# Optimization experiments

Measured on AMD Instinct MI355X. Metric: run time of the kernel, lower is better.

Reference implementation:

```python
import jax, jax.numpy as jnp
import numpy as np

N = 100000      # num nodes
E = 1600000     # num edges
F_IN = 128
F_OUT = 128
BN_EPS = 1e-5


def setup_inputs() -> dict:
    key = jax.random.key(0)
    ks = jax.random.split(key, 8)
    x = jax.random.normal(ks[0], (N, F_IN), dtype=jnp.float32)
    edge_index = jax.random.randint(ks[1], (2, E), 0, N, dtype=jnp.int64)
    # GIN learnable epsilon (init 0.0)
    eps = jnp.zeros((), dtype=jnp.float32)
    # MLP: Linear(F_IN->F_OUT) -> BatchNorm1d -> ReLU -> Linear(F_OUT->F_OUT)
    lim1 = 1.0 / np.sqrt(F_IN)
    W1 = jax.random.uniform(ks[2], (F_OUT, F_IN), minval=-lim1, maxval=lim1, dtype=jnp.float32)
    b1 = jax.random.uniform(ks[3], (F_OUT,), minval=-lim1, maxval=lim1, dtype=jnp.float32)
    gamma = jnp.ones((F_OUT,), dtype=jnp.float32)
    beta = jnp.zeros((F_OUT,), dtype=jnp.float32)
    lim2 = 1.0 / np.sqrt(F_OUT)
    W2 = jax.random.uniform(ks[4], (F_OUT, F_OUT), minval=-lim2, maxval=lim2, dtype=jnp.float32)
    b2 = jax.random.uniform(ks[5], (F_OUT,), minval=-lim2, maxval=lim2, dtype=jnp.float32)
    return {"x": x, "edge_index": edge_index, "eps": eps,
            "W1": W1, "b1": b1, "gamma": gamma, "beta": beta,
            "W2": W2, "b2": b2}


def reference(x, edge_index, eps, W1, b1, gamma, beta, W2, b2):
    row, col = edge_index[0], edge_index[1]
    # gather neighbor features and scatter-add into destination nodes
    agg = jax.ops.segment_sum(x[col], row, num_segments=x.shape[0])  # [N, F_IN]
    h = (1.0 + eps) * x + agg
    # Linear 1
    h = h @ W1.T + b1  # [N, F_OUT]
    # BatchNorm1d (training mode: batch stats over nodes, biased variance)
    mu = jnp.mean(h, axis=0)
    var = jnp.mean(jnp.square(h - mu), axis=0)
    h = (h - mu) * jax.lax.rsqrt(var + BN_EPS) * gamma + beta
    h = jax.nn.relu(h)
    # Linear 2
    return h @ W2.T + b2
```

## Files before the change

### kernel.cpp

```cpp
#include <hip/hip_runtime.h>


#define F 128
#define NPB 64

typedef __attribute__((ext_vector_type(8))) short short8;
typedef __attribute__((ext_vector_type(4))) float float4v;

__device__ inline float b2f(unsigned short u) {
    union { unsigned int i; float f; } v; v.i = ((unsigned int)u) << 16; return v.f;
}
__device__ inline unsigned short f2b(float f) {
    union { float f; unsigned int i; } v; v.f = f;
    unsigned int r = v.i + 0x7FFFu + ((v.i >> 16) & 1u);
    return (unsigned short)(r >> 16);
}

__global__ __launch_bounds__(256) void conv_kernel(const float* __restrict__ x,
                                                   unsigned short* __restrict__ xh, int total,
                                                   const float* __restrict__ W1,
                                                   const float* __restrict__ W2,
                                                   unsigned short* __restrict__ w1h,
                                                   unsigned short* __restrict__ w2h,
                                                   int* __restrict__ bucketCnt, int nbuk,
                                                   float* __restrict__ stats) {
    int t = blockIdx.x * 256 + threadIdx.x;
    int i = t * 8;
    if (i < total) {
        float4 v0 = *(const float4*)(x + i);
        float4 v1 = *(const float4*)(x + i + 4);
        short8 o;
        o[0] = (short)f2b(v0.x); o[1] = (short)f2b(v0.y); o[2] = (short)f2b(v0.z); o[3] = (short)f2b(v0.w);
        o[4] = (short)f2b(v1.x); o[5] = (short)f2b(v1.y); o[6] = (short)f2b(v1.z); o[7] = (short)f2b(v1.w);
        *(short8*)(xh + i) = o;
    }
    if (t < F * F) {
        w1h[t] = f2b(W1[t]);
        w2h[t] = f2b(W2[t]);
    }
    if (blockIdx.x == 0) {
        for (int k = threadIdx.x; k < nbuk; k += 256) bucketCnt[k] = 0;
    } else if (blockIdx.x == 1) {
        if (threadIdx.x < 256) stats[threadIdx.x] = 0.f;
    }
}

__global__ __launch_bounds__(256) void bucket_hist_kernel(const int* __restrict__ rows,
                                                          int* __restrict__ bucketCnt,
                                                          int E, int nbuk) {
    extern __shared__ int bh[];
    int tid = threadIdx.x;
    for (int i = tid; i < nbuk; i += 256) bh[i] = 0;
    __syncthreads();
    int stride = gridDim.x * 256;
    for (int i = blockIdx.x * 256 + tid; i < E; i += stride)
        atomicAdd(&bh[rows[i] >> 6], 1);
    __syncthreads();
    for (int b = tid; b < nbuk; b += 256) {
        int c = bh[b];
        if (c) atomicAdd(&bucketCnt[b], c);
    }
}

__global__ void scan_buckets_kernel(const int* __restrict__ bucketCnt, int* __restrict__ bOffs,
                                    int* __restrict__ gcursor, int nbuk) {
    const int SEG = 7;
    __shared__ int tmp[256];
    int t = threadIdx.x;
    int base = t * SEG;
    int v[SEG], s = 0;
#pragma unroll
    for (int j = 0; j < SEG; j++) {
        int idx = base + j;
        v[j] = (idx < nbuk) ? bucketCnt[idx] : 0;
        s += v[j];
    }
    tmp[t] = s;
    __syncthreads();
    for (int off = 1; off < 256; off <<= 1) {
        int u = (t >= off) ? tmp[t - off] : 0;
        __syncthreads();
        tmp[t] += u;
        __syncthreads();
    }
    int run = tmp[t] - s;
#pragma unroll
    for (int j = 0; j < SEG; j++) {
        int idx = base + j;
        if (idx < nbuk) { bOffs[idx] = run; gcursor[idx] = run; }
        run += v[j];
    }
    if (t == 255) bOffs[nbuk] = tmp[255];
}

__global__ __launch_bounds__(1024) void binned_scatter_kernel(const int* __restrict__ rows,
                                                              const int* __restrict__ cols,
                                                              int* __restrict__ gcursor,
                                                              int* __restrict__ recbuf,
                                                              int E, int nbuk) {
    extern __shared__ int sm[];
    int* bh = sm;
    int* gb = sm + nbuk;
    int tid = threadIdx.x;
    int chunk = (E + gridDim.x - 1) / gridDim.x;
    int e0 = blockIdx.x * chunk;
    int e1 = min(E, e0 + chunk);
    for (int i = tid; i < nbuk; i += 1024) bh[i] = 0;
    __syncthreads();
    for (int i = e0 + tid; i < e1; i += 1024)
        atomicAdd(&bh[rows[i] >> 6], 1);
    __syncthreads();
    for (int b = tid; b < nbuk; b += 1024) {
        int c = bh[b];
        gb[b] = c ? atomicAdd(&gcursor[b], c) : 0;
        bh[b] = 0;
    }
    __syncthreads();
    for (int i = e0 + tid; i < e1; i += 1024) {
        int r = rows[i], c = cols[i];
        int k = r >> 6;
        int rk = atomicAdd(&bh[k], 1);
        recbuf[gb[k] + rk] = (c << 6) | (r & 63);
    }
}

__global__ __launch_bounds__(256) void bucket_sort_kernel(const int* __restrict__ recbuf,
                                                          const int* __restrict__ bOffs,
                                                          int* __restrict__ clist,
                                                          int* __restrict__ offs,
                                                          int n, int nbuk) {
    __shared__ int hist[NPB];
    __shared__ int cur[NPB];
    int b = blockIdx.x, tid = threadIdx.x;
    int base = bOffs[b];
    int cnt = bOffs[b + 1] - base;
    if (tid < NPB) hist[tid] = 0;
    __syncthreads();
    for (int i = tid; i < cnt; i += 256) atomicAdd(&hist[recbuf[base + i] & 63], 1);
    __syncthreads();
    if (tid < 64) {
        int h = hist[tid], v = h;
#pragma unroll
        for (int off = 1; off < 64; off <<= 1) {
            int u = __shfl_up(v, off, 64);
            if (tid >= off) v += u;
        }
        cur[tid] = v - h;
        int g = b * NPB + tid;
        if (g < n) offs[g] = base + v - h;
    }
    if (b == 0 && tid == 0) offs[n] = bOffs[nbuk];
    __syncthreads();
    for (int i = tid; i < cnt; i += 256) {
        int r = recbuf[base + i];
        int p = atomicAdd(&cur[r & 63], 1);
        clist[base + p] = r >> 6;
    }
}

__global__ __launch_bounds__(256) void agg_kernel(const unsigned short* __restrict__ xh,
                                                  const int* __restrict__ offs,
                                                  const int* __restrict__ clist,
                                                  const float* __restrict__ epsPtr,
                                                  unsigned short* __restrict__ h0h, int n) {
    int wave = threadIdx.x >> 6, lane = threadIdx.x & 63;
    int node = blockIdx.x * 4 + wave;
    if (node >= n) return;
    int qt = lane >> 4;
    int c16 = lane & 15;
    const short8* xh8 = (const short8*)xh;
    float acc[8];
#pragma unroll
    for (int j = 0; j < 8; j++) acc[j] = 0.f;
    int s = offs[node], e = offs[node + 1];
    int i = s;
    for (; i + 16 <= e; i += 16) {
        int c[4];
#pragma unroll
        for (int u = 0; u < 4; u++) c[u] = clist[i + 4 * u + qt];
        short8 v[4];
#pragma unroll
        for (int u = 0; u < 4; u++) v[u] = xh8[(size_t)c[u] * 16 + c16];
#pragma unroll
        for (int u = 0; u < 4; u++)
#pragma unroll
            for (int j = 0; j < 8; j++) acc[j] += b2f((unsigned short)v[u][j]);
    }
    if (i < e) {
        int c[4];
#pragma unroll
        for (int u = 0; u < 4; u++) {
            int idx = i + 4 * u + qt;
            c[u] = (idx < e) ? clist[idx] : -1;
        }
        short8 v[4];
#pragma unroll
        for (int u = 0; u < 4; u++)
            v[u] = xh8[(size_t)(c[u] < 0 ? 0 : c[u]) * 16 + c16];
#pragma unroll
        for (int u = 0; u < 4; u++) {
            if (c[u] >= 0) {
#pragma unroll
                for (int j = 0; j < 8; j++) acc[j] += b2f((unsigned short)v[u][j]);
            }
        }
    }
#pragma unroll
    for (int j = 0; j < 8; j++) {
        acc[j] += __shfl_xor(acc[j], 16, 64);
        acc[j] += __shfl_xor(acc[j], 32, 64);
    }
    if (qt == 0) {
        float sc = 1.0f + epsPtr[0];
        short8 xv = xh8[(size_t)node * 16 + c16];
        short8 o;
#pragma unroll
        for (int j = 0; j < 8; j++) {
            float r = fmaf(sc, b2f((unsigned short)xv[j]), acc[j]);
            o[j] = (short)f2b(r);
        }
        ((short8*)h0h)[(size_t)node * 16 + c16] = o;
    }
}

#define WLD 136
__global__ __launch_bounds__(256, 2) void gemm1_mfma_kernel(const unsigned short* __restrict__ h0h,
                                                            const unsigned short* __restrict__ w1h,
                                                            const float* __restrict__ b1,
                                                            unsigned short* __restrict__ h1h,
                                                            float* __restrict__ stats, int n) {
    __shared__ unsigned short wl[128 * WLD];
    __shared__ float red[4 * 256];
    int tid = threadIdx.x;
    for (int i = tid; i < 128 * 16; i += 256) {
        int r = i >> 4, ch = i & 15;
        *(short8*)(wl + r * WLD + ch * 8) = *(const short8*)(w1h + r * 128 + ch * 8);
    }
    __syncthreads();

    int wv = tid >> 6, lane = tid & 63;
    int q = lane >> 4, c15 = lane & 15;
    int rowbase = blockIdx.x * 64 + wv * 16;
    int arow = rowbase + c15; if (arow >= n) arow = n - 1;
    const unsigned short* aptr = h0h + (size_t)arow * 128 + q * 8;

    float4v acc[8];
#pragma unroll
    for (int nt = 0; nt < 8; nt++) {
        float bb = b1[nt * 16 + c15];
        acc[nt] = (float4v){bb, bb, bb, bb};
    }
#pragma unroll
    for (int ks = 0; ks < 4; ks++) {
        short8 a = *(const short8*)(aptr + ks * 32);
        const unsigned short* wp = wl + q * 8 + ks * 32;
#pragma unroll
        for (int nt = 0; nt < 8; nt++) {
            short8 b = *(const short8*)(wp + (nt * 16 + c15) * WLD);
            acc[nt] = __builtin_amdgcn_mfma_f32_16x16x32_bf16(a, b, acc[nt], 0, 0, 0);
        }
    }

    float sum[8], sq[8];
#pragma unroll
    for (int nt = 0; nt < 8; nt++) {
        sum[nt] = 0.f; sq[nt] = 0.f;
#pragma unroll
        for (int r = 0; r < 4; r++) {
            int row = rowbase + q * 4 + r;
            if (row < n) {
                float v = acc[nt][r];
                h1h[(size_t)row * 128 + nt * 16 + c15] = f2b(v);
                sum[nt] += v; sq[nt] += v * v;
            }
        }
        sum[nt] += __shfl_xor(sum[nt], 16, 64);
        sum[nt] += __shfl_xor(sum[nt], 32, 64);
        sq[nt]  += __shfl_xor(sq[nt], 16, 64);
        sq[nt]  += __shfl_xor(sq[nt], 32, 64);
    }
    if (lane < 16) {
#pragma unroll
        for (int nt = 0; nt < 8; nt++) {
            red[wv * 256 + nt * 16 + c15] = sum[nt];
            red[wv * 256 + 128 + nt * 16 + c15] = sq[nt];
        }
    }
    __syncthreads();
    if (wv == 0) {
        for (int c = lane; c < 128; c += 64) {
            float S = red[c] + red[256 + c] + red[512 + c] + red[768 + c];
            float Q = red[128 + c] + red[384 + c] + red[640 + c] + red[896 + c];
            atomicAdd(&stats[c], S);
            atomicAdd(&stats[128 + c], Q);
        }
    }
}

__global__ __launch_bounds__(256, 2) void gemm2_mfma_kernel(const unsigned short* __restrict__ h1h,
                                                            const unsigned short* __restrict__ w2h,
                                                            const float* __restrict__ b2,
                                                            const float* __restrict__ stats,
                                                            const float* __restrict__ gamma,
                                                            const float* __restrict__ beta,
                                                            float* __restrict__ out, int n) {
    __shared__ unsigned short wl[128 * WLD];
    __shared__ float ssl[256];
    int tid = threadIdx.x;
    for (int i = tid; i < 128 * 16; i += 256) {
        int r = i >> 4, ch = i & 15;
        *(short8*)(wl + r * WLD + ch * 8) = *(const short8*)(w2h + r * 128 + ch * 8);
    }
    if (tid < 128) {
        float inv_n = 1.0f / (float)n;
        float mu = stats[tid] * inv_n;
        float var = stats[F + tid] * inv_n - mu * mu;
        var = fmaxf(var, 0.0f);
        float rs = rsqrtf(var + 1e-5f);
        float s = gamma[tid] * rs;
        ssl[tid] = s;
        ssl[F + tid] = beta[tid] - mu * s;
    }
    __syncthreads();

    int wv = tid >> 6, lane = tid & 63;
    int q = lane >> 4, c15 = lane & 15;
    int rowbase = blockIdx.x * 64 + wv * 16;
    int arow = rowbase + c15; if (arow >= n) arow = n - 1;
    const unsigned short* aptr = h1h + (size_t)arow * 128 + q * 8;

    float4v acc[8];
#pragma unroll
    for (int nt = 0; nt < 8; nt++) {
        float bb = b2[nt * 16 + c15];
        acc[nt] = (float4v){bb, bb, bb, bb};
    }
#pragma unroll
    for (int ks = 0; ks < 4; ks++) {
        short8 araw = *(const short8*)(aptr + ks * 32);
        const float* ssp = ssl + ks * 32 + q * 8;
        float4 s0 = *(const float4*)(ssp);
        float4 s1 = *(const float4*)(ssp + 4);
        float4 t0 = *(const float4*)(ssp + 128);
        float4 t1 = *(const float4*)(ssp + 132);
        short8 a;
        a[0] = (short)f2b(fmaxf(fmaf(b2f((unsigned short)araw[0]), s0.x, t0.x), 0.f));
        a[1] = (short)f2b(fmaxf(fmaf(b2f((unsigned short)araw[1]), s0.y, t0.y), 0.f));
        a[2] = (short)f2b(fmaxf(fmaf(b2f((unsigned short)araw[2]), s0.z, t0.z), 0.f));
        a[3] = (short)f2b(fmaxf(fmaf(b2f((unsigned short)araw[3]), s0.w, t0.w), 0.f));
        a[4] = (short)f2b(fmaxf(fmaf(b2f((unsigned short)araw[4]), s1.x, t1.x), 0.f));
        a[5] = (short)f2b(fmaxf(fmaf(b2f((unsigned short)araw[5]), s1.y, t1.y), 0.f));
        a[6] = (short)f2b(fmaxf(fmaf(b2f((unsigned short)araw[6]), s1.z, t1.z), 0.f));
        a[7] = (short)f2b(fmaxf(fmaf(b2f((unsigned short)araw[7]), s1.w, t1.w), 0.f));
        const unsigned short* wp = wl + q * 8 + ks * 32;
#pragma unroll
        for (int nt = 0; nt < 8; nt++) {
            short8 b = *(const short8*)(wp + (nt * 16 + c15) * WLD);
            acc[nt] = __builtin_amdgcn_mfma_f32_16x16x32_bf16(a, b, acc[nt], 0, 0, 0);
        }
    }
#pragma unroll
    for (int nt = 0; nt < 8; nt++) {
#pragma unroll
        for (int r = 0; r < 4; r++) {
            int row = rowbase + q * 4 + r;
            if (row < n)
                out[(size_t)row * 128 + nt * 16 + c15] = acc[nt][r];
        }
    }
}

extern "C" void kernel_launch(void* const* d_in, const int* in_sizes, int n_in,
                              void* d_out, int out_size, void* d_ws, size_t ws_size,
                              hipStream_t stream) {
    const float* x     = (const float*)d_in[0];
    const int*   ei    = (const int*)d_in[1];
    const float* eps   = (const float*)d_in[2];
    const float* W1    = (const float*)d_in[3];
    const float* b1    = (const float*)d_in[4];
    const float* gamma = (const float*)d_in[5];
    const float* beta  = (const float*)d_in[6];
    const float* W2    = (const float*)d_in[7];
    const float* b2    = (const float*)d_in[8];
    float* out = (float*)d_out;

    const int E = in_sizes[1] / 2;
    const int n = in_sizes[0] / F;
    const int nbuk = (n + NPB - 1) / NPB;

    char* w = (char*)d_ws;
    auto alloc = [&](size_t bytes) -> void* {
        void* p = (void*)w;
        w += (bytes + 255) & ~(size_t)255;
        return p;
    };
    int*            bucketCnt = (int*)alloc((size_t)nbuk * 4);
    int*            bOffs     = (int*)alloc((size_t)(nbuk + 1) * 4);
    int*            gcursor   = (int*)alloc((size_t)nbuk * 4);
    int*            offs      = (int*)alloc((size_t)(n + 1) * 4);
    float*          stats     = (float*)alloc(256 * 4);
    unsigned short* w1h       = (unsigned short*)alloc(F * F * 2);
    unsigned short* w2h       = (unsigned short*)alloc(F * F * 2);
    int*            recbuf    = (int*)alloc((size_t)E * 4);
    int*            clist     = (int*)alloc((size_t)E * 4);
    unsigned short* xh        = (unsigned short*)alloc((size_t)n * F * 2);
    unsigned short* h0h       = (unsigned short*)alloc((size_t)n * F * 2);
    unsigned short* h1h       = (unsigned short*)alloc((size_t)n * F * 2);

    const int* rows = ei;
    const int* cols = ei + E;

    conv_kernel<<<(n * F / 8 + 255) / 256, 256, 0, stream>>>(x, xh, n * F, W1, W2, w1h, w2h,
                                                             bucketCnt, nbuk, stats);
    bucket_hist_kernel<<<256, 256, nbuk * 4, stream>>>(rows, bucketCnt, E, nbuk);
    scan_buckets_kernel<<<1, 256, 0, stream>>>(bucketCnt, bOffs, gcursor, nbuk);
    binned_scatter_kernel<<<128, 1024, nbuk * 8, stream>>>(rows, cols, gcursor, recbuf, E, nbuk);
    bucket_sort_kernel<<<nbuk, 256, 0, stream>>>(recbuf, bOffs, clist, offs, n, nbuk);
    agg_kernel<<<(n + 3) / 4, 256, 0, stream>>>(xh, offs, clist, eps, h0h, n);

    int ntiles = (n + 63) / 64;
    gemm1_mfma_kernel<<<ntiles, 256, 0, stream>>>(h0h, w1h, b1, h1h, stats, n);
    gemm2_mfma_kernel<<<ntiles, 256, 0, stream>>>(h1h, w2h, b2, stats, gamma, beta, out, n);
}
```

Measured before the change: 296.8 us.

## Fuse per-bucket sort with neighbor aggregation using LDS column lists

Merges the bucket sort and aggregation kernels so each 64-node bucket sorts its edge records into a shared-memory column list and immediately aggregates those nodes. This removes one launch and the global round trip of the sorted column list and offsets. Buckets larger than the LDS capacity fall back to a global list. Grid sizes of the histogram and scatter kernels are also enlarged. The catch is that aggregation parallelism drops to four waves per 64 nodes, and the larger LDS footprint may lower occupancy.

```diff
diff --git a/kernel.cpp b/kernel.cpp
--- a/kernel.cpp
+++ b/kernel.cpp
@@ -3,6 +3,7 @@
 
 #define F 128
 #define NPB 64
+#define CLCAP 3072
 
 typedef __attribute__((ext_vector_type(8))) short short8;
 typedef __attribute__((ext_vector_type(4))) float float4v;
@@ -124,13 +125,17 @@
     }
 }
 
-__global__ __launch_bounds__(256) void bucket_sort_kernel(const int* __restrict__ recbuf,
-                                                          const int* __restrict__ bOffs,
-                                                          int* __restrict__ clist,
-                                                          int* __restrict__ offs,
-                                                          int n, int nbuk) {
+__global__ __launch_bounds__(256) void sort_agg_kernel(const int* __restrict__ recbuf,
+                                                       const int* __restrict__ bOffs,
+                                                       const unsigned short* __restrict__ xh,
+                                                       const float* __restrict__ epsPtr,
+                                                       unsigned short* __restrict__ h0h,
+                                                       int* __restrict__ clist,
+                                                       int n, int nbuk) {
     __shared__ int hist[NPB];
     __shared__ int cur[NPB];
+    __shared__ int offs_s[NPB + 1];
+    __shared__ int cl[CLCAP];
     int b = blockIdx.x, tid = threadIdx.x;
     int base = bOffs[b];
     int cnt = bOffs[b + 1] - base;
@@ -146,80 +151,89 @@
             if (tid >= off) v += u;
         }
         cur[tid] = v - h;
-        int g = b * NPB + tid;
-        if (g < n) offs[g] = base + v - h;
-    }
-    if (b == 0 && tid == 0) offs[n] = bOffs[nbuk];
-    __syncthreads();
-    for (int i = tid; i < cnt; i += 256) {
-        int r = recbuf[base + i];
-        int p = atomicAdd(&cur[r & 63], 1);
-        clist[base + p] = r >> 6;
-    }
-}
-
-__global__ __launch_bounds__(256) void agg_kernel(const unsigned short* __restrict__ xh,
-                                                  const int* __restrict__ offs,
-                                                  const int* __restrict__ clist,
-                                                  const float* __restrict__ epsPtr,
-                                                  unsigned short* __restrict__ h0h, int n) {
-    int wave = threadIdx.x >> 6, lane = threadIdx.x & 63;
-    int node = blockIdx.x * 4 + wave;
-    if (node >= n) return;
+        offs_s[tid] = v - h;
+        if (tid == 63) offs_s[64] = v;
+    }
+    __syncthreads();
+    bool inlds = (cnt <= CLCAP);
+    if (inlds) {
+        for (int i = tid; i < cnt; i += 256) {
+            int r = recbuf[base + i];
+            int p = atomicAdd(&cur[r & 63], 1);
+            cl[p] = r >> 6;
+        }
+    } else {
+        for (int i = tid; i < cnt; i += 256) {
+            int r = recbuf[base + i];
+            int p = atomicAdd(&cur[r & 63], 1);
+            clist[base + p] = r >> 6;
+        }
+    }
+    __syncthreads();
+
+    int wv = tid >> 6, lane = tid & 63;
     int qt = lane >> 4;
     int c16 = lane & 15;
     const short8* xh8 = (const short8*)xh;
-    float acc[8];
-#pragma unroll
-    for (int j = 0; j < 8; j++) acc[j] = 0.f;
-    int s = offs[node], e = offs[node + 1];
-    int i = s;
-    for (; i + 16 <= e; i += 16) {
-        int c[4];
-#pragma unroll
-        for (int u = 0; u < 4; u++) c[u] = clist[i + 4 * u + qt];
-        short8 v[4];
-#pragma unroll
-        for (int u = 0; u < 4; u++) v[u] = xh8[(size_t)c[u] * 16 + c16];
-#pragma unroll
-        for (int u = 0; u < 4; u++)
-#pragma unroll
-            for (int j = 0; j < 8; j++) acc[j] += b2f((unsigned short)v[u][j]);
-    }
-    if (i < e) {
-        int c[4];
-#pragma unroll
-        for (int u = 0; u < 4; u++) {
-            int idx = i + 4 * u + qt;
-            c[u] = (idx < e) ? clist[idx] : -1;
-        }
-        short8 v[4];
-#pragma unroll
-        for (int u = 0; u < 4; u++)
-            v[u] = xh8[(size_t)(c[u] < 0 ? 0 : c[u]) * 16 + c16];
-#pragma unroll
-        for (int u = 0; u < 4; u++) {
-            if (c[u] >= 0) {
+    float sc = 1.0f + epsPtr[0];
+    const int* glist = clist + base;
+    for (int nd = wv; nd < NPB; nd += 4) {
+        int node = b * NPB + nd;
+        if (node >= n) break;
+        int s = offs_s[nd], e = offs_s[nd + 1];
+        float acc[8];
+#pragma unroll
+        for (int j = 0; j < 8; j++) acc[j] = 0.f;
+        int i = s;
+        for (; i + 16 <= e; i += 16) {
+            int c[4];
+#pragma unroll
+            for (int u = 0; u < 4; u++) {
+                int idx = i + 4 * u + qt;
+                c[u] = inlds ? cl[idx] : glist[idx];
+            }
+            short8 v[4];
+#pragma unroll
+            for (int u = 0; u < 4; u++) v[u] = xh8[(size_t)c[u] * 16 + c16];
+#pragma unroll
+            for (int u = 0; u < 4; u++)
 #pragma unroll
                 for (int j = 0; j < 8; j++) acc[j] += b2f((unsigned short)v[u][j]);
+        }
+        if (i < e) {
+            int c[4];
+#pragma unroll
+            for (int u = 0; u < 4; u++) {
+                int idx = i + 4 * u + qt;
+                c[u] = (idx < e) ? (inlds ? cl[idx] : glist[idx]) : -1;
             }
-        }
-    }
-#pragma unroll
-    for (int j = 0; j < 8; j++) {
-        acc[j] += __shfl_xor(acc[j], 16, 64);
-        acc[j] += __shfl_xor(acc[j], 32, 64);
-    }
-    if (qt == 0) {
-        float sc = 1.0f + epsPtr[0];
-        short8 xv = xh8[(size_t)node * 16 + c16];
-        short8 o;
+            short8 v[4];
+#pragma unroll
+            for (int u = 0; u < 4; u++)
+                v[u] = xh8[(size_t)(c[u] < 0 ? 0 : c[u]) * 16 + c16];
+#pragma unroll
+            for (int u = 0; u < 4; u++) {
+                if (c[u] >= 0) {
+#pragma unroll
+                    for (int j = 0; j < 8; j++) acc[j] += b2f((unsigned short)v[u][j]);
+                }
+            }
+        }
 #pragma unroll
         for (int j = 0; j < 8; j++) {
-            float r = fmaf(sc, b2f((unsigned short)xv[j]), acc[j]);
-            o[j] = (short)f2b(r);
-        }
-        ((short8*)h0h)[(size_t)node * 16 + c16] = o;
+            acc[j] += __shfl_xor(acc[j], 16, 64);
+            acc[j] += __shfl_xor(acc[j], 32, 64);
+        }
+        if (qt == 0) {
+            short8 xv = xh8[(size_t)node * 16 + c16];
+            short8 o;
+#pragma unroll
+            for (int j = 0; j < 8; j++) {
+                float r = fmaf(sc, b2f((unsigned short)xv[j]), acc[j]);
+                o[j] = (short)f2b(r);
+            }
+            ((short8*)h0h)[(size_t)node * 16 + c16] = o;
+        }
     }
 }
 
@@ -397,7 +411,6 @@
     int*            bucketCnt = (int*)alloc((size_t)nbuk * 4);
     int*            bOffs     = (int*)alloc((size_t)(nbuk + 1) * 4);
     int*            gcursor   = (int*)alloc((size_t)nbuk * 4);
-    int*            offs      = (int*)alloc((size_t)(n + 1) * 4);
     float*          stats     = (float*)alloc(256 * 4);
     unsigned short* w1h       = (unsigned short*)alloc(F * F * 2);
     unsigned short* w2h       = (unsigned short*)alloc(F * F * 2);
@@ -412,11 +425,10 @@
 
     conv_kernel<<<(n * F / 8 + 255) / 256, 256, 0, stream>>>(x, xh, n * F, W1, W2, w1h, w2h,
                                                              bucketCnt, nbuk, stats);
-    bucket_hist_kernel<<<256, 256, nbuk * 4, stream>>>(rows, bucketCnt, E, nbuk);
+    bucket_hist_kernel<<<512, 256, nbuk * 4, stream>>>(rows, bucketCnt, E, nbuk);
     scan_buckets_kernel<<<1, 256, 0, stream>>>(bucketCnt, bOffs, gcursor, nbuk);
-    binned_scatter_kernel<<<128, 1024, nbuk * 8, stream>>>(rows, cols, gcursor, recbuf, E, nbuk);
-    bucket_sort_kernel<<<nbuk, 256, 0, stream>>>(recbuf, bOffs, clist, offs, n, nbuk);
-    agg_kernel<<<(n + 3) / 4, 256, 0, stream>>>(xh, offs, clist, eps, h0h, n);
+    binned_scatter_kernel<<<384, 1024, nbuk * 8, stream>>>(rows, cols, gcursor, recbuf, E, nbuk);
+    sort_agg_kernel<<<nbuk, 256, 0, stream>>>(recbuf, bOffs, xh, eps, h0h, clist, n, nbuk);
 
     int ntiles = (n + 63) / 64;
     gemm1_mfma_kernel<<<ntiles, 256, 0, stream>>>(h0h, w1h, b1, h1h, stats, n);
```

Result: no change. 297.5 us (+0.2%).
